# Performance work log

Hardware: AMD Instinct MI355X
Metric: run time of the kernel (lower is better)

Reference implementation:

```python
import jax, jax.numpy as jnp
import numpy as np

HEAD_SIZE = 64
N_EMBD = 768

def setup_inputs() -> dict:
    key = jax.random.key(0)
    kx, kq, kk, kv = jax.random.split(key, 4)
    x = jax.random.normal(kx, (4, 4096, N_EMBD), dtype=jnp.float32)
    s = 1.0 / np.sqrt(N_EMBD)
    Wq = jax.random.normal(kq, (N_EMBD, HEAD_SIZE), dtype=jnp.float32) * s
    Wk = jax.random.normal(kk, (N_EMBD, HEAD_SIZE), dtype=jnp.float32) * s
    Wv = jax.random.normal(kv, (N_EMBD, HEAD_SIZE), dtype=jnp.float32) * s
    return {"x": x, "Wq": Wq, "Wk": Wk, "Wv": Wv}

def reference(x, Wq, Wk, Wv):
    b, t, c = x.shape
    h = Wq.shape[1]
    q = jnp.einsum('btc,ch->bth', x, Wq)
    k = jnp.einsum('btc,ch->bth', x, Wk)
    v = jnp.einsum('btc,ch->bth', x, Wv)
    scores = jnp.einsum('bqh,bkh->bqk', q, k) / jnp.sqrt(jnp.float32(h))
    causal = jnp.tril(jnp.ones((t, t), dtype=bool))  # [t,t]
    scores = jnp.where(causal, scores, -jnp.inf)
    attn = jax.nn.softmax(scores, axis=-1)
    return jnp.einsum('bqk,bkh->bqh', attn, v)
```

## Files before the change

kernel.cpp:

```cpp
#include <hip/hip_runtime.h>
#include <math.h>

#define BB 4
#define TT 4096
#define CC 768
#define HH 64
#define NN 192
#define LDP 72
#define GR 32
#define BKK 64

typedef __bf16 bf16x8 __attribute__((ext_vector_type(8)));
typedef float floatx4 __attribute__((ext_vector_type(4)));
typedef unsigned short u16x8 __attribute__((ext_vector_type(8)));

__device__ inline unsigned short f2bf(float f) {
    union { __bf16 b; unsigned short u; } v;
    v.b = (__bf16)f;
    return v.u;
}

__global__ __launch_bounds__(256) void wprep(const float* __restrict__ Wq,
                                             const float* __restrict__ Wk,
                                             const float* __restrict__ Wv,
                                             unsigned short* __restrict__ wtf) {
    const int idx = blockIdx.x * 256 + threadIdx.x;
    if (idx >= NN * CC) return;
    const int j = idx & 7;
    const int lane = (idx >> 3) & 63;
    const int rest = idx >> 9;
    const int kg = rest % 24;
    const int n_tile = rest / 24;
    const int c = kg * 32 + (lane >> 4) * 8 + j;
    const int n = n_tile * 16 + (lane & 15);
    const float* W = (n < 64) ? Wq : (n < 128) ? Wk : Wv;
    wtf[idx] = f2bf(W[c * HH + (n & 63)]);
}

__global__ __launch_bounds__(256) void qkv_gemm(const float* __restrict__ x,
                                                const unsigned short* __restrict__ wtf,
                                                unsigned short* __restrict__ qb,
                                                unsigned short* __restrict__ kb,
                                                unsigned short* __restrict__ vbt) {
    __shared__ unsigned short As[GR * LDP];

    const int tid = threadIdx.x;
    const int w = tid >> 6, lane = tid & 63;
    const int l15 = lane & 15, quad = lane >> 4;
    const int m0 = blockIdx.x * GR;
    const int n0 = w * 48;
    const int nt0 = w * 3;

    const int ar = tid >> 3;
    const int akoff = (tid & 7) * 8;
    const float* xp = x + (size_t)(m0 + ar) * CC + akoff;

    floatx4 acc[2][3] = {};

    float4 pa0 = *(const float4*)(xp);
    float4 pa1 = *(const float4*)(xp + 4);

    for (int step = 0; step < 12; ++step) {
        __syncthreads();
        u16x8 pk;
        pk[0] = f2bf(pa0.x); pk[1] = f2bf(pa0.y);
        pk[2] = f2bf(pa0.z); pk[3] = f2bf(pa0.w);
        pk[4] = f2bf(pa1.x); pk[5] = f2bf(pa1.y);
        pk[6] = f2bf(pa1.z); pk[7] = f2bf(pa1.w);
        *(u16x8*)(As + ar * LDP + akoff) = pk;
        __syncthreads();

        if (step < 11) {
            pa0 = *(const float4*)(xp + (step + 1) * BKK);
            pa1 = *(const float4*)(xp + (step + 1) * BKK + 4);
        }

        bf16x8 a0[2], a1[2];
#pragma unroll
        for (int rg = 0; rg < 2; ++rg) {
            a0[rg] = *(const bf16x8*)(As + (16 * rg + l15) * LDP + quad * 8);
            a1[rg] = *(const bf16x8*)(As + (16 * rg + l15) * LDP + 32 + quad * 8);
        }
#pragma unroll
        for (int j = 0; j < 3; ++j) {
            const unsigned short* bp =
                wtf + ((size_t)((nt0 + j) * 24 + 2 * step) * 64 + lane) * 8;
            const bf16x8 b0 = *(const bf16x8*)(bp);
            const bf16x8 b1 = *(const bf16x8*)(bp + 512);
#pragma unroll
            for (int rg = 0; rg < 2; ++rg) {
                acc[rg][j] = __builtin_amdgcn_mfma_f32_16x16x32_bf16(a0[rg], b0, acc[rg][j], 0, 0, 0);
                acc[rg][j] = __builtin_amdgcn_mfma_f32_16x16x32_bf16(a1[rg], b1, acc[rg][j], 0, 0, 0);
            }
        }
    }

    const int b = m0 >> 12;
#pragma unroll
    for (int j = 0; j < 3; ++j) {
        const int n = n0 + j * 16 + l15;
        const int mid = n >> 6;
        const int h = n & 63;
#pragma unroll
        for (int rg = 0; rg < 2; ++rg) {
            const int tloc = (m0 & (TT - 1)) + 16 * rg + quad * 4;
            if (mid == 2) {
                ushort4 pk;
                pk.x = f2bf(acc[rg][j][0]); pk.y = f2bf(acc[rg][j][1]);
                pk.z = f2bf(acc[rg][j][2]); pk.w = f2bf(acc[rg][j][3]);
                *(ushort4*)(vbt + ((size_t)b * HH + h) * TT + tloc) = pk;
            } else {
                unsigned short* dst = (mid == 0) ? qb : kb;
#pragma unroll
                for (int r = 0; r < 4; ++r)
                    dst[(size_t)(m0 + 16 * rg + quad * 4 + r) * HH + h] = f2bf(acc[rg][j][r]);
            }
        }
    }
}

template<int CH>
__global__ __launch_bounds__(256) void attn_part(const unsigned short* __restrict__ qb,
                                                 const unsigned short* __restrict__ kb,
                                                 const unsigned short* __restrict__ vbt,
                                                 float* __restrict__ Opart,
                                                 float* __restrict__ lsum) {
    __shared__ unsigned short Ks[64 * LDP];
    __shared__ unsigned short VTs[64 * LDP];
    __shared__ unsigned short Ps[4][16 * LDP];

    constexpr int NG = 64 / CH;
    constexpr int TOTB = CH * (NG * (NG + 1)) / 2;

    const int b = blockIdx.x & 3;
    int rem = TOTB - 1 - (blockIdx.x >> 2);
    int g = 0;
    while (rem >= CH * (g + 1)) { rem -= CH * (g + 1); ++g; }
    const int qt = g * CH + rem / (g + 1);
    const int ch = rem - (rem / (g + 1)) * (g + 1);

    const int q0  = qt * 64;
    const int tid = threadIdx.x;
    const int w = tid >> 6, lane = tid & 63;
    const int l15 = lane & 15, quad = lane >> 4;

    const unsigned short* Qb  = qb  + (size_t)b * TT * HH;
    const unsigned short* Kb  = kb  + (size_t)b * TT * HH;
    const unsigned short* VTb = vbt + (size_t)b * HH * TT;

    const int qrow = q0 + 16 * w + l15;
    const bf16x8 qf0 = *(const bf16x8*)(Qb + (size_t)qrow * HH + quad * 8);
    const bf16x8 qf1 = *(const bf16x8*)(Qb + (size_t)qrow * HH + 32 + quad * 8);

    floatx4 O[4] = {};
    floatx4 lacc = {0.f, 0.f, 0.f, 0.f};

    const int kt0 = ch * CH;
    const int kt1 = min(kt0 + CH, qt + 1);
    for (int kt = kt0; kt < kt1; ++kt) {
        __syncthreads();
        const unsigned short* Kt = Kb + (size_t)(kt * 64) * HH;
        const unsigned short* Vt = VTb + kt * 64;
#pragma unroll
        for (int e = 0; e < 2; ++e) {
            const int chunk = tid + 256 * e;
            const int r = chunk >> 3, c0 = (chunk & 7) * 8;
            *(u16x8*)(Ks + r * LDP + c0)  = *(const u16x8*)(Kt + r * HH + c0);
            *(u16x8*)(VTs + r * LDP + c0) = *(const u16x8*)(Vt + (size_t)r * TT + c0);
        }
        __syncthreads();

        floatx4 s[4];
#pragma unroll
        for (int ki = 0; ki < 4; ++ki) {
            const bf16x8 kf0 = *(const bf16x8*)(Ks + (16 * ki + l15) * LDP + quad * 8);
            const bf16x8 kf1 = *(const bf16x8*)(Ks + (16 * ki + l15) * LDP + 32 + quad * 8);
            floatx4 c = {};
            c = __builtin_amdgcn_mfma_f32_16x16x32_bf16(qf0, kf0, c, 0, 0, 0);
            c = __builtin_amdgcn_mfma_f32_16x16x32_bf16(qf1, kf1, c, 0, 0, 0);
            s[ki] = c * 0.125f;
        }

        if (kt == qt) {
#pragma unroll
            for (int ki = 0; ki < 4; ++ki)
#pragma unroll
                for (int r = 0; r < 4; ++r) {
                    const int kloc = 16 * ki + l15;
                    const int qloc = 16 * w + quad * 4 + r;
                    if (kloc > qloc) s[ki][r] = -INFINITY;
                }
        }

#pragma unroll
        for (int ki = 0; ki < 4; ++ki)
#pragma unroll
            for (int r = 0; r < 4; ++r) {
                const float p = __expf(s[ki][r]);
                s[ki][r] = p;
                lacc[r] += p;
            }

        unsigned short* Pw = Ps[w];
#pragma unroll
        for (int ki = 0; ki < 4; ++ki)
#pragma unroll
            for (int r = 0; r < 4; ++r)
                Pw[(quad * 4 + r) * LDP + 16 * ki + l15] = f2bf(s[ki][r]);

        const bf16x8 pf0 = *(const bf16x8*)(Pw + l15 * LDP + quad * 8);
        const bf16x8 pf1 = *(const bf16x8*)(Pw + l15 * LDP + 32 + quad * 8);
#pragma unroll
        for (int di = 0; di < 4; ++di) {
            const bf16x8 vf0 = *(const bf16x8*)(VTs + (16 * di + l15) * LDP + quad * 8);
            const bf16x8 vf1 = *(const bf16x8*)(VTs + (16 * di + l15) * LDP + 32 + quad * 8);
            O[di] = __builtin_amdgcn_mfma_f32_16x16x32_bf16(pf0, vf0, O[di], 0, 0, 0);
            O[di] = __builtin_amdgcn_mfma_f32_16x16x32_bf16(pf1, vf1, O[di], 0, 0, 0);
        }
    }

    float l_r[4];
#pragma unroll
    for (int r = 0; r < 4; ++r) {
        float v = lacc[r];
#pragma unroll
        for (int msk = 8; msk >= 1; msk >>= 1) v += __shfl_xor(v, msk, 64);
        l_r[r] = v;
    }

    const int pbase = ((b * 64 + qt) * NG + ch) * 64;
    float* Op = Opart + (size_t)pbase * HH + 16 * w * HH;
#pragma unroll
    for (int di = 0; di < 4; ++di)
#pragma unroll
        for (int r = 0; r < 4; ++r)
            Op[(quad * 4 + r) * HH + 16 * di + l15] = O[di][r];
    if (l15 == 0) {
#pragma unroll
        for (int r = 0; r < 4; ++r)
            lsum[pbase + 16 * w + quad * 4 + r] = l_r[r];
    }
}

template<int CH>
__global__ __launch_bounds__(256) void attn_merge(const float* __restrict__ Opart,
                                                  const float* __restrict__ lsum,
                                                  float* __restrict__ out) {
    constexpr int NG = 64 / CH;
    const int g = blockIdx.x * 256 + threadIdx.x;
    const int row = g >> 6, d = g & 63;
    const int b = row >> 12, t = row & (TT - 1);
    const int qt = t >> 6, rloc = t & 63;
    const int nchunk = qt / CH + 1;
    const int pbase = ((b * 64 + qt) * NG) * 64 + rloc;

    float O = 0.f, L = 0.f;
#pragma unroll 4
    for (int c = 0; c < nchunk; ++c) {
        const int idx = pbase + c * 64;
        L += lsum[idx];
        O += Opart[(size_t)idx * HH + d];
    }
    out[(size_t)row * HH + d] = O / L;
}

__global__ __launch_bounds__(256) void attn_full(const unsigned short* __restrict__ qb,
                                                 const unsigned short* __restrict__ kb,
                                                 const unsigned short* __restrict__ vbt,
                                                 float* __restrict__ out) {
    __shared__ unsigned short Ks[64 * LDP];
    __shared__ unsigned short VTs[64 * LDP];
    __shared__ unsigned short Ps[4][16 * LDP];

    const int b   = blockIdx.x >> 6;
    const int qt  = blockIdx.x & 63;
    const int q0  = qt * 64;
    const int tid = threadIdx.x;
    const int w = tid >> 6, lane = tid & 63;
    const int l15 = lane & 15, quad = lane >> 4;

    const unsigned short* Qb  = qb  + (size_t)b * TT * HH;
    const unsigned short* Kb  = kb  + (size_t)b * TT * HH;
    const unsigned short* VTb = vbt + (size_t)b * HH * TT;

    const int qrow = q0 + 16 * w + l15;
    const bf16x8 qf0 = *(const bf16x8*)(Qb + (size_t)qrow * HH + quad * 8);
    const bf16x8 qf1 = *(const bf16x8*)(Qb + (size_t)qrow * HH + 32 + quad * 8);

    floatx4 O[4] = {};
    floatx4 lacc = {0.f, 0.f, 0.f, 0.f};

    for (int kt = 0; kt <= qt; ++kt) {
        __syncthreads();
        const unsigned short* Kt = Kb + (size_t)(kt * 64) * HH;
        const unsigned short* Vt = VTb + kt * 64;
#pragma unroll
        for (int e = 0; e < 2; ++e) {
            const int chunk = tid + 256 * e;
            const int r = chunk >> 3, c0 = (chunk & 7) * 8;
            *(u16x8*)(Ks + r * LDP + c0)  = *(const u16x8*)(Kt + r * HH + c0);
            *(u16x8*)(VTs + r * LDP + c0) = *(const u16x8*)(Vt + (size_t)r * TT + c0);
        }
        __syncthreads();

        floatx4 s[4];
#pragma unroll
        for (int ki = 0; ki < 4; ++ki) {
            const bf16x8 kf0 = *(const bf16x8*)(Ks + (16 * ki + l15) * LDP + quad * 8);
            const bf16x8 kf1 = *(const bf16x8*)(Ks + (16 * ki + l15) * LDP + 32 + quad * 8);
            floatx4 c = {};
            c = __builtin_amdgcn_mfma_f32_16x16x32_bf16(qf0, kf0, c, 0, 0, 0);
            c = __builtin_amdgcn_mfma_f32_16x16x32_bf16(qf1, kf1, c, 0, 0, 0);
            s[ki] = c * 0.125f;
        }
        if (kt == qt) {
#pragma unroll
            for (int ki = 0; ki < 4; ++ki)
#pragma unroll
                for (int r = 0; r < 4; ++r)
                    if (16 * ki + l15 > 16 * w + quad * 4 + r) s[ki][r] = -INFINITY;
        }
#pragma unroll
        for (int ki = 0; ki < 4; ++ki)
#pragma unroll
            for (int r = 0; r < 4; ++r) {
                const float p = __expf(s[ki][r]);
                s[ki][r] = p; lacc[r] += p;
            }

        unsigned short* Pw = Ps[w];
#pragma unroll
        for (int ki = 0; ki < 4; ++ki)
#pragma unroll
            for (int r = 0; r < 4; ++r)
                Pw[(quad * 4 + r) * LDP + 16 * ki + l15] = f2bf(s[ki][r]);

        const bf16x8 pf0 = *(const bf16x8*)(Pw + l15 * LDP + quad * 8);
        const bf16x8 pf1 = *(const bf16x8*)(Pw + l15 * LDP + 32 + quad * 8);
#pragma unroll
        for (int di = 0; di < 4; ++di) {
            const bf16x8 vf0 = *(const bf16x8*)(VTs + (16 * di + l15) * LDP + quad * 8);
            const bf16x8 vf1 = *(const bf16x8*)(VTs + (16 * di + l15) * LDP + 32 + quad * 8);
            O[di] = __builtin_amdgcn_mfma_f32_16x16x32_bf16(pf0, vf0, O[di], 0, 0, 0);
            O[di] = __builtin_amdgcn_mfma_f32_16x16x32_bf16(pf1, vf1, O[di], 0, 0, 0);
        }
    }
    float l_r[4];
#pragma unroll
    for (int r = 0; r < 4; ++r) {
        float v = lacc[r];
#pragma unroll
        for (int msk = 8; msk >= 1; msk >>= 1) v += __shfl_xor(v, msk, 64);
        l_r[r] = v;
    }
    float* outp = out + ((size_t)b * TT + q0 + 16 * w) * HH;
#pragma unroll
    for (int di = 0; di < 4; ++di)
#pragma unroll
        for (int r = 0; r < 4; ++r)
            outp[(quad * 4 + r) * HH + 16 * di + l15] = O[di][r] / l_r[r];
}

extern "C" void kernel_launch(void* const* d_in, const int* in_sizes, int n_in,
                              void* d_out, int out_size, void* d_ws, size_t ws_size,
                              hipStream_t stream) {
    const float* x  = (const float*)d_in[0];
    const float* Wq = (const float*)d_in[1];
    const float* Wk = (const float*)d_in[2];
    const float* Wv = (const float*)d_in[3];
    float* out = (float*)d_out;

    const size_t nQKV = (size_t)BB * TT * HH;
    unsigned short* qb  = (unsigned short*)d_ws;
    unsigned short* kb  = qb + nQKV;
    unsigned short* vbt = kb + nQKV;
    unsigned short* wtf = vbt + nQKV;
    float* Opart = (float*)(wtf + (size_t)NN * CC);

    const size_t prows8  = (size_t)BB * 64 * 8 * 64;
    const size_t prows16 = (size_t)BB * 64 * 4 * 64;
    float* lsum8  = Opart + prows8 * HH;
    float* lsum16 = Opart + prows16 * HH;
    const size_t need8  = (size_t)((char*)(lsum8  + prows8)  - (char*)d_ws);
    const size_t need16 = (size_t)((char*)(lsum16 + prows16) - (char*)d_ws);

    wprep<<<(NN * CC + 255) / 256, 256, 0, stream>>>(Wq, Wk, Wv, wtf);
    qkv_gemm<<<(BB * TT) / GR, 256, 0, stream>>>(x, wtf, qb, kb, vbt);
    if (ws_size >= need8) {
        attn_part<8><<<BB * 288, 256, 0, stream>>>(qb, kb, vbt, Opart, lsum8);
        attn_merge<8><<<(BB * TT * HH) / 256, 256, 0, stream>>>(Opart, lsum8, out);
    } else if (ws_size >= need16) {
        attn_part<16><<<BB * 160, 256, 0, stream>>>(qb, kb, vbt, Opart, lsum16);
        attn_merge<16><<<(BB * TT * HH) / 256, 256, 0, stream>>>(Opart, lsum16, out);
    } else {
        attn_full<<<BB * (TT / 64), 256, 0, stream>>>(qb, kb, vbt, out);
    }
}
```

Measured before the change: 131.9 us.

## Stage full x row tile in LDS and give each attention wave two query row groups

```diff
diff --git a/kernel.cpp b/kernel.cpp
--- a/kernel.cpp
+++ b/kernel.cpp
@@ -8,7 +8,7 @@
 #define NN 192
 #define LDP 72
 #define GR 32
-#define BKK 64
+#define XSTR 776
 
 typedef __bf16 bf16x8 __attribute__((ext_vector_type(8)));
 typedef float floatx4 __attribute__((ext_vector_type(4)));
@@ -42,7 +42,7 @@
                                                 unsigned short* __restrict__ qb,
                                                 unsigned short* __restrict__ kb,
                                                 unsigned short* __restrict__ vbt) {
-    __shared__ unsigned short As[GR * LDP];
+    __shared__ unsigned short As[GR * XSTR];
 
     const int tid = threadIdx.x;
     const int w = tid >> 6, lane = tid & 63;
@@ -51,35 +51,29 @@
     const int n0 = w * 48;
     const int nt0 = w * 3;
 
-    const int ar = tid >> 3;
-    const int akoff = (tid & 7) * 8;
-    const float* xp = x + (size_t)(m0 + ar) * CC + akoff;
+    const float* xbase = x + (size_t)m0 * CC;
+#pragma unroll
+    for (int e = 0; e < 12; ++e) {
+        const int c = tid + 256 * e;
+        const int r = c / 96, off = (c - r * 96) * 8;
+        const float4 v0 = *(const float4*)(xbase + (size_t)c * 8);
+        const float4 v1 = *(const float4*)(xbase + (size_t)c * 8 + 4);
+        u16x8 pk;
+        pk[0] = f2bf(v0.x); pk[1] = f2bf(v0.y); pk[2] = f2bf(v0.z); pk[3] = f2bf(v0.w);
+        pk[4] = f2bf(v1.x); pk[5] = f2bf(v1.y); pk[6] = f2bf(v1.z); pk[7] = f2bf(v1.w);
+        *(u16x8*)(As + r * XSTR + off) = pk;
+    }
+    __syncthreads();
 
     floatx4 acc[2][3] = {};
-
-    float4 pa0 = *(const float4*)(xp);
-    float4 pa1 = *(const float4*)(xp + 4);
-
+#pragma unroll 4
     for (int step = 0; step < 12; ++step) {
-        __syncthreads();
-        u16x8 pk;
-        pk[0] = f2bf(pa0.x); pk[1] = f2bf(pa0.y);
-        pk[2] = f2bf(pa0.z); pk[3] = f2bf(pa0.w);
-        pk[4] = f2bf(pa1.x); pk[5] = f2bf(pa1.y);
-        pk[6] = f2bf(pa1.z); pk[7] = f2bf(pa1.w);
-        *(u16x8*)(As + ar * LDP + akoff) = pk;
-        __syncthreads();
-
-        if (step < 11) {
-            pa0 = *(const float4*)(xp + (step + 1) * BKK);
-            pa1 = *(const float4*)(xp + (step + 1) * BKK + 4);
-        }
-
         bf16x8 a0[2], a1[2];
 #pragma unroll
         for (int rg = 0; rg < 2; ++rg) {
-            a0[rg] = *(const bf16x8*)(As + (16 * rg + l15) * LDP + quad * 8);
-            a1[rg] = *(const bf16x8*)(As + (16 * rg + l15) * LDP + 32 + quad * 8);
+            const unsigned short* ap = As + (16 * rg + l15) * XSTR + step * 64 + quad * 8;
+            a0[rg] = *(const bf16x8*)(ap);
+            a1[rg] = *(const bf16x8*)(ap + 32);
         }
 #pragma unroll
         for (int j = 0; j < 3; ++j) {
@@ -120,14 +114,14 @@
 }
 
 template<int CH>
-__global__ __launch_bounds__(256) void attn_part(const unsigned short* __restrict__ qb,
+__global__ __launch_bounds__(128) void attn_part(const unsigned short* __restrict__ qb,
                                                  const unsigned short* __restrict__ kb,
                                                  const unsigned short* __restrict__ vbt,
                                                  float* __restrict__ Opart,
                                                  float* __restrict__ lsum) {
     __shared__ unsigned short Ks[64 * LDP];
     __shared__ unsigned short VTs[64 * LDP];
-    __shared__ unsigned short Ps[4][16 * LDP];
+    __shared__ unsigned short Ps[2][32 * LDP];
 
     constexpr int NG = 64 / CH;
     constexpr int TOTB = CH * (NG * (NG + 1)) / 2;
@@ -148,12 +142,16 @@
     const unsigned short* Kb  = kb  + (size_t)b * TT * HH;
     const unsigned short* VTb = vbt + (size_t)b * HH * TT;
 
-    const int qrow = q0 + 16 * w + l15;
-    const bf16x8 qf0 = *(const bf16x8*)(Qb + (size_t)qrow * HH + quad * 8);
-    const bf16x8 qf1 = *(const bf16x8*)(Qb + (size_t)qrow * HH + 32 + quad * 8);
-
-    floatx4 O[4] = {};
-    floatx4 lacc = {0.f, 0.f, 0.f, 0.f};
+    bf16x8 qf0[2], qf1[2];
+#pragma unroll
+    for (int rg = 0; rg < 2; ++rg) {
+        const unsigned short* qp = Qb + (size_t)(q0 + 32 * w + 16 * rg + l15) * HH + quad * 8;
+        qf0[rg] = *(const bf16x8*)(qp);
+        qf1[rg] = *(const bf16x8*)(qp + 32);
+    }
+
+    floatx4 O[2][4] = {};
+    floatx4 lacc[2] = {};
 
     const int kt0 = ch * CH;
     const int kt1 = min(kt0 + CH, qt + 1);
@@ -162,83 +160,104 @@
         const unsigned short* Kt = Kb + (size_t)(kt * 64) * HH;
         const unsigned short* Vt = VTb + kt * 64;
 #pragma unroll
-        for (int e = 0; e < 2; ++e) {
-            const int chunk = tid + 256 * e;
+        for (int e = 0; e < 4; ++e) {
+            const int chunk = tid + 128 * e;
             const int r = chunk >> 3, c0 = (chunk & 7) * 8;
             *(u16x8*)(Ks + r * LDP + c0)  = *(const u16x8*)(Kt + r * HH + c0);
             *(u16x8*)(VTs + r * LDP + c0) = *(const u16x8*)(Vt + (size_t)r * TT + c0);
         }
         __syncthreads();
 
-        floatx4 s[4];
+        floatx4 s[2][4];
 #pragma unroll
         for (int ki = 0; ki < 4; ++ki) {
-            const bf16x8 kf0 = *(const bf16x8*)(Ks + (16 * ki + l15) * LDP + quad * 8);
-            const bf16x8 kf1 = *(const bf16x8*)(Ks + (16 * ki + l15) * LDP + 32 + quad * 8);
-            floatx4 c = {};
-            c = __builtin_amdgcn_mfma_f32_16x16x32_bf16(qf0, kf0, c, 0, 0, 0);
-            c = __builtin_amdgcn_mfma_f32_16x16x32_bf16(qf1, kf1, c, 0, 0, 0);
-            s[ki] = c * 0.125f;
+            const unsigned short* kp = Ks + (16 * ki + l15) * LDP + quad * 8;
+            const bf16x8 kf0 = *(const bf16x8*)(kp);
+            const bf16x8 kf1 = *(const bf16x8*)(kp + 32);
+#pragma unroll
+            for (int rg = 0; rg < 2; ++rg) {
+                floatx4 c = {};
+                c = __builtin_amdgcn_mfma_f32_16x16x32_bf16(qf0[rg], kf0, c, 0, 0, 0);
+                c = __builtin_amdgcn_mfma_f32_16x16x32_bf16(qf1[rg], kf1, c, 0, 0, 0);
+                s[rg][ki] = c * 0.125f;
+            }
         }
 
         if (kt == qt) {
 #pragma unroll
+            for (int rg = 0; rg < 2; ++rg)
+#pragma unroll
+                for (int ki = 0; ki < 4; ++ki)
+#pragma unroll
+                    for (int r = 0; r < 4; ++r) {
+                        const int kloc = 16 * ki + l15;
+                        const int qloc = 32 * w + 16 * rg + quad * 4 + r;
+                        if (kloc > qloc) s[rg][ki][r] = -INFINITY;
+                    }
+        }
+
+#pragma unroll
+        for (int rg = 0; rg < 2; ++rg)
+#pragma unroll
             for (int ki = 0; ki < 4; ++ki)
 #pragma unroll
                 for (int r = 0; r < 4; ++r) {
-                    const int kloc = 16 * ki + l15;
-                    const int qloc = 16 * w + quad * 4 + r;
-                    if (kloc > qloc) s[ki][r] = -INFINITY;
+                    const float p = __expf(s[rg][ki][r]);
+                    s[rg][ki][r] = p;
+                    lacc[rg][r] += p;
                 }
-        }
-
-#pragma unroll
-        for (int ki = 0; ki < 4; ++ki)
-#pragma unroll
-            for (int r = 0; r < 4; ++r) {
-                const float p = __expf(s[ki][r]);
-                s[ki][r] = p;
-                lacc[r] += p;
+
+        unsigned short* Pw = Ps[w];
+#pragma unroll
+        for (int rg = 0; rg < 2; ++rg)
+#pragma unroll
+            for (int ki = 0; ki < 4; ++ki)
+#pragma unroll
+                for (int r = 0; r < 4; ++r)
+                    Pw[(16 * rg + quad * 4 + r) * LDP + 16 * ki + l15] = f2bf(s[rg][ki][r]);
+
+        bf16x8 pf0[2], pf1[2];
+#pragma unroll
+        for (int rg = 0; rg < 2; ++rg) {
+            const unsigned short* pp = Pw + (16 * rg + l15) * LDP + quad * 8;
+            pf0[rg] = *(const bf16x8*)(pp);
+            pf1[rg] = *(const bf16x8*)(pp + 32);
+        }
+#pragma unroll
+        for (int di = 0; di < 4; ++di) {
+            const unsigned short* vp = VTs + (16 * di + l15) * LDP + quad * 8;
+            const bf16x8 vf0 = *(const bf16x8*)(vp);
+            const bf16x8 vf1 = *(const bf16x8*)(vp + 32);
+#pragma unroll
+            for (int rg = 0; rg < 2; ++rg) {
+                O[rg][di] = __builtin_amdgcn_mfma_f32_16x16x32_bf16(pf0[rg], vf0, O[rg][di], 0, 0, 0);
+                O[rg][di] = __builtin_amdgcn_mfma_f32_16x16x32_bf16(pf1[rg], vf1, O[rg][di], 0, 0, 0);
             }
-
-        unsigned short* Pw = Ps[w];
-#pragma unroll
-        for (int ki = 0; ki < 4; ++ki)
+        }
+    }
+
+    const int pbase = ((b * 64 + qt) * NG + ch) * 64;
+#pragma unroll
+    for (int rg = 0; rg < 2; ++rg) {
+        float l_r[4];
+#pragma unroll
+        for (int r = 0; r < 4; ++r) {
+            float v = lacc[rg][r];
+#pragma unroll
+            for (int msk = 8; msk >= 1; msk >>= 1) v += __shfl_xor(v, msk, 64);
+            l_r[r] = v;
+        }
+        float* Op = Opart + (size_t)(pbase + 32 * w + 16 * rg) * HH;
+#pragma unroll
+        for (int di = 0; di < 4; ++di)
 #pragma unroll
             for (int r = 0; r < 4; ++r)
-                Pw[(quad * 4 + r) * LDP + 16 * ki + l15] = f2bf(s[ki][r]);
-
-        const bf16x8 pf0 = *(const bf16x8*)(Pw + l15 * LDP + quad * 8);
-        const bf16x8 pf1 = *(const bf16x8*)(Pw + l15 * LDP + 32 + quad * 8);
-#pragma unroll
-        for (int di = 0; di < 4; ++di) {
-            const bf16x8 vf0 = *(const bf16x8*)(VTs + (16 * di + l15) * LDP + quad * 8);
-            const bf16x8 vf1 = *(const bf16x8*)(VTs + (16 * di + l15) * LDP + 32 + quad * 8);
-            O[di] = __builtin_amdgcn_mfma_f32_16x16x32_bf16(pf0, vf0, O[di], 0, 0, 0);
-            O[di] = __builtin_amdgcn_mfma_f32_16x16x32_bf16(pf1, vf1, O[di], 0, 0, 0);
-        }
-    }
-
-    float l_r[4];
-#pragma unroll
-    for (int r = 0; r < 4; ++r) {
-        float v = lacc[r];
-#pragma unroll
-        for (int msk = 8; msk >= 1; msk >>= 1) v += __shfl_xor(v, msk, 64);
-        l_r[r] = v;
-    }
-
-    const int pbase = ((b * 64 + qt) * NG + ch) * 64;
-    float* Op = Opart + (size_t)pbase * HH + 16 * w * HH;
-#pragma unroll
-    for (int di = 0; di < 4; ++di)
-#pragma unroll
-        for (int r = 0; r < 4; ++r)
-            Op[(quad * 4 + r) * HH + 16 * di + l15] = O[di][r];
-    if (l15 == 0) {
-#pragma unroll
-        for (int r = 0; r < 4; ++r)
-            lsum[pbase + 16 * w + quad * 4 + r] = l_r[r];
+                Op[(quad * 4 + r) * HH + 16 * di + l15] = O[rg][di][r];
+        if (l15 == 0) {
+#pragma unroll
+            for (int r = 0; r < 4; ++r)
+                lsum[pbase + 32 * w + 16 * rg + quad * 4 + r] = l_r[r];
+        }
     }
 }
 
@@ -387,10 +406,10 @@
     wprep<<<(NN * CC + 255) / 256, 256, 0, stream>>>(Wq, Wk, Wv, wtf);
     qkv_gemm<<<(BB * TT) / GR, 256, 0, stream>>>(x, wtf, qb, kb, vbt);
     if (ws_size >= need8) {
-        attn_part<8><<<BB * 288, 256, 0, stream>>>(qb, kb, vbt, Opart, lsum8);
+        attn_part<8><<<BB * 288, 128, 0, stream>>>(qb, kb, vbt, Opart, lsum8);
         attn_merge<8><<<(BB * TT * HH) / 256, 256, 0, stream>>>(Opart, lsum8, out);
     } else if (ws_size >= need16) {
-        attn_part<16><<<BB * 160, 256, 0, stream>>>(qb, kb, vbt, Opart, lsum16);
+        attn_part<16><<<BB * 160, 128, 0, stream>>>(qb, kb, vbt, Opart, lsum16);
         attn_merge<16><<<(BB * TT * HH) / 256, 256, 0, stream>>>(Opart, lsum16, out);
     } else {
         attn_full<<<BB * (TT / 64), 256, 0, stream>>>(qb, kb, vbt, out);
```

Measured after the change: 134.2 us. Within noise of the previous version (+1.7%).
